# Optimization experiments

Measured on AMD Instinct MI355X. Metric: run time of the kernel, lower is better.

The kernel has to match this reference:

```python
import jax, jax.numpy as jnp
import numpy as np
from jax import lax

N_CHANNELS = 64
N_FILTERS = 256
N_LAYERS = 9  # residual blocks use dilations 2**1 .. 2**(N_LAYERS-1)


def causal_conv1d(x, w, dilation):
    """Causal dilated conv. x: [B,T,Cin], w: [K,Cin,Cout]."""
    pad = (w.shape[0] - 1) * dilation
    return lax.conv_general_dilated(
        x, w, window_strides=(1,), padding=[(pad, 0)],
        rhs_dilation=(dilation,), dimension_numbers=("NWC", "WIO", "NWC"))


def setup_inputs() -> dict:
    key = jax.random.key(0)
    ks = jax.random.split(key, 12)
    B, T, C, F, L = 8, 4096, N_CHANNELS, N_FILTERS, N_LAYERS
    s = lambda fan_in: 1.0 / np.sqrt(fan_in)
    return {
        "x": jax.random.normal(ks[0], (B, T, C), jnp.float32),
        "Wc": jax.random.normal(ks[1], (2, C, F), jnp.float32) * s(2 * C),
        "Wf": jax.random.normal(ks[2], (L - 1, 2, F, F), jnp.float32) * s(2 * F),
        "Wg": jax.random.normal(ks[3], (L - 1, 2, F, F), jnp.float32) * s(2 * F),
        "Wr": jax.random.normal(ks[4], (L - 1, F, F), jnp.float32) * s(F),
        "br": jnp.zeros((L - 1, F), jnp.float32),
        "Ws": jax.random.normal(ks[5], (L - 1, F, F), jnp.float32) * s(F),
        "bs": jnp.zeros((L - 1, F), jnp.float32),
        "Wd1": jax.random.normal(ks[6], (F, C), jnp.float32) * s(F),
        "bd1": jnp.zeros((C,), jnp.float32),
        "Wd2": jax.random.normal(ks[7], (C, C), jnp.float32) * s(C),
        "bd2": jnp.zeros((C,), jnp.float32),
    }


def reference(x, Wc, Wf, Wg, Wr, br, Ws, bs, Wd1, bd1, Wd2, bd2):
    # Initial causal conv, dilation 1, no bias.
    out = causal_conv1d(x, Wc, 1)  # [B,T,F]
    skip_sum = jnp.zeros_like(out)
    for i in range(N_LAYERS - 1):
        d = 2 ** (i + 1)
        f = causal_conv1d(out, Wf[i], d)
        g = causal_conv1d(out, Wg[i], d)
        z = jnp.tanh(f) * jax.nn.sigmoid(g)
        out = out + jnp.einsum("btf,fo->bto", z, Wr[i]) + br[i]
        skip_sum = skip_sum + jnp.einsum("btf,fo->bto", z, Ws[i]) + bs[i]
    h = jax.nn.selu(skip_sum)
    h = jnp.einsum("btf,fc->btc", h, Wd1) + bd1
    h = jax.nn.selu(h)
    h = jnp.einsum("btc,co->bto", h, Wd2) + bd2
    return h
```

## Files before the change

kernel.cpp:

```cpp
#include <hip/hip_runtime.h>
#include <cstdint>

typedef unsigned short u16;
typedef unsigned int u32;
typedef __attribute__((ext_vector_type(8))) short s8v;
typedef __attribute__((ext_vector_type(4))) float f4v;

#define FCH 256

__device__ __forceinline__ float bf2f(u16 u){ return __uint_as_float(((u32)u)<<16); }
__device__ __forceinline__ u16 f2bf(float x){
  u32 u = __float_as_uint(x);
  u += 0x7fffu + ((u>>16)&1u);
  return (u16)(u>>16);
}
__device__ __forceinline__ float rcpf(float x){ return __builtin_amdgcn_rcpf(x); }
__device__ __forceinline__ uint4 pack8(float4 a, float4 b){
  uint4 o;
  o.x = (u32)f2bf(a.x) | ((u32)f2bf(a.y)<<16);
  o.y = (u32)f2bf(a.z) | ((u32)f2bf(a.w)<<16);
  o.z = (u32)f2bf(b.x) | ((u32)f2bf(b.y)<<16);
  o.w = (u32)f2bf(b.z) | ((u32)f2bf(b.w)<<16);
  return o;
}
__device__ __forceinline__ float seluf(float x){
  const float sc = 1.0507009873554805f, al = 1.6732632423543772f;
  return x > 0.f ? sc*x : sc*al*(__expf(x)-1.f);
}
__device__ __forceinline__ s8v ldmask(const u16* p, u32 m){
  uint4 r = *reinterpret_cast<const uint4*>(p);
  r.x &= m; r.y &= m; r.z &= m; r.w &= m;
  s8v v; *reinterpret_cast<uint4*>(&v) = r;
  return v;
}
__device__ __forceinline__ int xcd_tile(int bid, int nT8){
  return nT8 ? ((bid & 7) * nT8 + (bid >> 3)) : bid;
}

__global__ __launch_bounds__(256) void pack_kernel(
    const float* __restrict__ Wc, const float* __restrict__ Wf, const float* __restrict__ Wg,
    const float* __restrict__ Wr, const float* __restrict__ Ws,
    const float* __restrict__ Wd1, const float* __restrict__ Wd2,
    u16* __restrict__ Bp1, u16* __restrict__ Bp2, u16* __restrict__ Bp0,
    u16* __restrict__ BpD1, u16* __restrict__ BpD2)
{
  int gid = blockIdx.x*256 + threadIdx.x;
  int frag = gid >> 6;
  int lane = gid & 63;
  int q = lane >> 4, i15 = lane & 15;
  u16 v[8];
  u16* dst;
  if (frag < 4096) {
    int layer = frag >> 9, rem = frag & 511;
    int kc = rem >> 5, nt = rem & 31;
    int n = nt*16 + i15;
    const float* W = (n < 256) ? Wf : Wg;
    int nn = (n < 256) ? n : n - 256;
    #pragma unroll
    for (int j = 0; j < 8; ++j) {
      int k = kc*32 + q*8 + j;
      int tap = k >> 8, cin = k & 255;
      v[j] = f2bf(W[((size_t)((layer*2 + tap)*256 + cin))*256 + nn]);
    }
    dst = Bp1 + (size_t)frag*512 + lane*8;
  } else if (frag < 6144) {
    int f = frag - 4096;
    int layer = f >> 8, rem = f & 255;
    int kc = rem >> 5, nt = rem & 31;
    int n = nt*16 + i15;
    const float* W = (n < 256) ? Wr : Ws;
    int nn = (n < 256) ? n : n - 256;
    #pragma unroll
    for (int j = 0; j < 8; ++j) {
      int k = kc*32 + q*8 + j;
      v[j] = f2bf(W[((size_t)(layer*256 + k))*256 + nn]);
    }
    dst = Bp2 + (size_t)f*512 + lane*8;
  } else if (frag < 6208) {
    int f = frag - 6144;
    int kc = f >> 4, nt = f & 15;
    int n = nt*16 + i15;
    #pragma unroll
    for (int j = 0; j < 8; ++j) {
      int k = kc*32 + q*8 + j;
      int tap = k >> 6, cin = k & 63;
      v[j] = f2bf(Wc[(size_t)(tap*64 + cin)*256 + n]);
    }
    dst = Bp0 + (size_t)f*512 + lane*8;
  } else if (frag < 6240) {
    int f = frag - 6208;
    int kc = f >> 2, nt = f & 3;
    int n = nt*16 + i15;
    #pragma unroll
    for (int j = 0; j < 8; ++j) {
      int k = kc*32 + q*8 + j;
      v[j] = f2bf(Wd1[(size_t)k*64 + n]);
    }
    dst = BpD1 + (size_t)f*512 + lane*8;
  } else if (frag < 6248) {
    int f = frag - 6240;
    int kc = f >> 2, nt = f & 3;
    int n = nt*16 + i15;
    #pragma unroll
    for (int j = 0; j < 8; ++j) {
      int k = kc*32 + q*8 + j;
      v[j] = f2bf(Wd2[(size_t)k*64 + n]);
    }
    dst = BpD2 + (size_t)f*512 + lane*8;
  } else return;
  uint4 o;
  o.x = (u32)v[0] | ((u32)v[1] << 16);
  o.y = (u32)v[2] | ((u32)v[3] << 16);
  o.z = (u32)v[4] | ((u32)v[5] << 16);
  o.w = (u32)v[6] | ((u32)v[7] << 16);
  *reinterpret_cast<uint4*>(dst) = o;
}

__global__ __launch_bounds__(256, 2) void conv0_kernel(
    const float* __restrict__ x, u16* __restrict__ outBf,
    const u16* __restrict__ Bp0, int nT8)
{
  __shared__ __align__(16) u16 ldsA[2][2048];
  const int tid = threadIdx.x;
  const int w = tid >> 6, lane = tid & 63, q = lane >> 4, i15 = lane & 15;
  const int rb = xcd_tile(blockIdx.x, nT8) * 64;
  const int sm = tid >> 2, sg = tid & 3;
  const int grow = rb + sm;
  const int tpos = grow & 4095;
  const int sunit = ((sm >> 4)*64 + sg*16 + ((sm & 15) ^ (sg << 1))) * 8;
  const int runit = (q*16 + (i15 ^ (q << 1))) * 8;

  f4v acc[4][4];
  #pragma unroll
  for (int jj = 0; jj < 4; ++jj)
    #pragma unroll
    for (int mt = 0; mt < 4; ++mt)
      acc[jj][mt] = (f4v){0.f,0.f,0.f,0.f};

  float4 f0 = {0.f,0.f,0.f,0.f}, f1 = {0.f,0.f,0.f,0.f};
  if (tpos >= 1) {
    const float* px = x + (size_t)(grow-1)*64 + sg*8;
    f0 = *reinterpret_cast<const float4*>(px);
    f1 = *reinterpret_cast<const float4*>(px + 4);
  }
  *reinterpret_cast<uint4*>(&ldsA[0][sunit]) = pack8(f0, f1);
  s8v bcur[4], bnxt[4];
  #pragma unroll
  for (int jj = 0; jj < 4; ++jj)
    bcur[jj] = *reinterpret_cast<const s8v*>(Bp0 + ((size_t)(w + 4*jj)*64 + lane)*8);
  __syncthreads();

  for (int kc = 0; kc < 4; ++kc) {
    const int cur = kc & 1;
    uint4 an = {0u,0u,0u,0u};
    if (kc < 3) {
      int kg = (kc+1)*32 + sg*8;
      int tap = kg >> 6, col = kg & 63;
      float4 g0 = {0.f,0.f,0.f,0.f}, g1 = {0.f,0.f,0.f,0.f};
      if (tap) {
        const float* px = x + (size_t)grow*64 + col;
        g0 = *reinterpret_cast<const float4*>(px);
        g1 = *reinterpret_cast<const float4*>(px + 4);
      } else if (tpos >= 1) {
        const float* px = x + (size_t)(grow-1)*64 + col;
        g0 = *reinterpret_cast<const float4*>(px);
        g1 = *reinterpret_cast<const float4*>(px + 4);
      }
      an = pack8(g0, g1);
      #pragma unroll
      for (int jj = 0; jj < 4; ++jj)
        bnxt[jj] = *reinterpret_cast<const s8v*>(Bp0 + (((size_t)(kc+1)*16 + (w + 4*jj))*64 + lane)*8);
    }
    s8v af[4];
    #pragma unroll
    for (int mt = 0; mt < 4; ++mt)
      af[mt] = *reinterpret_cast<const s8v*>(&ldsA[cur][mt*512 + runit]);
    #pragma unroll
    for (int jj = 0; jj < 4; ++jj)
      #pragma unroll
      for (int mt = 0; mt < 4; ++mt)
        acc[jj][mt] = __builtin_amdgcn_mfma_f32_16x16x32_bf16(af[mt], bcur[jj], acc[jj][mt], 0,0,0);
    if (kc < 3) {
      *reinterpret_cast<uint4*>(&ldsA[cur ^ 1][sunit]) = an;
      #pragma unroll
      for (int jj = 0; jj < 4; ++jj) bcur[jj] = bnxt[jj];
    }
    __syncthreads();
  }

  #pragma unroll
  for (int jj = 0; jj < 4; ++jj) {
    const int cc = (w + 4*jj)*16 + i15;
    #pragma unroll
    for (int mt = 0; mt < 4; ++mt)
      #pragma unroll
      for (int r = 0; r < 4; ++r) {
        const int g2 = rb + mt*16 + q*4 + r;
        outBf[(size_t)g2*FCH + cc] = f2bf(acc[jj][mt][r]);
      }
  }
}

__global__ __launch_bounds__(256, 3) void layer_kernel(
    const u16* __restrict__ inBf, u16* __restrict__ outBf,
    u16* __restrict__ skipB,
    const u16* __restrict__ Bp1, const u16* __restrict__ Bp2,
    const float* __restrict__ br, const float* __restrict__ bs,
    int dil, int first, int nT8)
{
  __shared__ __align__(16) u16 ldsZ[32*264];
  const int tid = threadIdx.x;
  const int w = __builtin_amdgcn_readfirstlane(tid >> 6);
  const int lane = tid & 63, q = lane >> 4, i15 = lane & 15;
  const int rb = xcd_tile(blockIdx.x, nT8) * 32;

  f4v acc[8][2];
  #pragma unroll
  for (int jj = 0; jj < 8; ++jj)
    #pragma unroll
    for (int mt = 0; mt < 2; ++mt)
      acc[jj][mt] = (f4v){0.f,0.f,0.f,0.f};

  {
    const u16* a0p[2];
    const u16* a1p[2];
    u32 am[2];
    #pragma unroll
    for (int mt = 0; mt < 2; ++mt) {
      const int row = rb + mt*16 + i15;
      const bool v = (row & 4095) >= dil;
      a0p[mt] = inBf + (size_t)(v ? row - dil : row)*FCH + q*8;
      a1p[mt] = inBf + (size_t)row*FCH + q*8;
      am[mt]  = v ? 0xffffffffu : 0u;
    }

    s8v bb[3][4], aa[4][2];
    #pragma unroll
    for (int j2 = 0; j2 < 4; ++j2) {
      bb[0][j2] = *reinterpret_cast<const s8v*>(Bp1 + ((size_t)(w + 4*j2)*64 + lane)*8);
      bb[1][j2] = *reinterpret_cast<const s8v*>(Bp1 + ((size_t)(w + 16 + 4*j2)*64 + lane)*8);
    }
    #pragma unroll
    for (int c = 0; c < 3; ++c)
      #pragma unroll
      for (int mt = 0; mt < 2; ++mt)
        aa[c][mt] = ldmask(a0p[mt] + c*32, am[mt]);

    #pragma unroll
    for (int s = 0; s < 32; ++s) {
      const int kc = s >> 1, h = s & 1;
      if (s + 2 < 32) {
        const int sp = s + 2, kcp = sp >> 1, hp = sp & 1;
        #pragma unroll
        for (int j2 = 0; j2 < 4; ++j2)
          bb[sp % 3][j2] = *reinterpret_cast<const s8v*>(
              Bp1 + (((size_t)kcp*32 + (w + 16*hp + 4*j2))*64 + lane)*8);
      }
      if (h == 0 && kc + 3 < 16) {
        const int ca = kc + 3;
        if (ca < 8) {
          #pragma unroll
          for (int mt = 0; mt < 2; ++mt)
            aa[ca & 3][mt] = ldmask(a0p[mt] + ca*32, am[mt]);
        } else {
          #pragma unroll
          for (int mt = 0; mt < 2; ++mt)
            aa[ca & 3][mt] = *reinterpret_cast<const s8v*>(a1p[mt] + (ca - 8)*32);
        }
      }
      __builtin_amdgcn_s_setprio(1);
      #pragma unroll
      for (int j2 = 0; j2 < 4; ++j2)
        #pragma unroll
        for (int mt = 0; mt < 2; ++mt)
          acc[h*4 + j2][mt] = __builtin_amdgcn_mfma_f32_16x16x32_bf16(
              aa[kc & 3][mt], bb[s % 3][j2], acc[h*4 + j2][mt], 0,0,0);
      __builtin_amdgcn_s_setprio(0);
    }
  }

  s8v s2b[3][4];
  #pragma unroll
  for (int j2 = 0; j2 < 4; ++j2) {
    s2b[0][j2] = *reinterpret_cast<const s8v*>(Bp2 + ((size_t)(w + 4*j2)*64 + lane)*8);
    s2b[1][j2] = *reinterpret_cast<const s8v*>(Bp2 + ((size_t)(w + 16 + 4*j2)*64 + lane)*8);
  }

  #pragma unroll
  for (int jj = 0; jj < 4; ++jj) {
    const int colb = (w + 4*jj)*16 + i15;
    #pragma unroll
    for (int mt = 0; mt < 2; ++mt)
      #pragma unroll
      for (int r = 0; r < 4; ++r) {
        float f = acc[jj][mt][r];
        float g = acc[jj+4][mt][r];
        float z = (1.f - 2.f*rcpf(__expf(2.f*f) + 1.f)) * rcpf(1.f + __expf(-g));
        ldsZ[(mt*16 + q*4 + r)*264 + colb] = f2bf(z);
      }
  }
  #pragma unroll
  for (int jj = 0; jj < 8; ++jj)
    #pragma unroll
    for (int mt = 0; mt < 2; ++mt)
      acc[jj][mt] = (f4v){0.f,0.f,0.f,0.f};
  __syncthreads();

  {
    s8v zf[2][2];
    #pragma unroll
    for (int mt = 0; mt < 2; ++mt)
      zf[0][mt] = *reinterpret_cast<const s8v*>(&ldsZ[(mt*16 + i15)*264 + q*8]);
    #pragma unroll
    for (int s = 0; s < 16; ++s) {
      const int kc = s >> 1, h = s & 1;
      if (s + 2 < 16) {
        const int sp = s + 2, kcp = sp >> 1, hp = sp & 1;
        #pragma unroll
        for (int j2 = 0; j2 < 4; ++j2)
          s2b[sp % 3][j2] = *reinterpret_cast<const s8v*>(
              Bp2 + (((size_t)kcp*32 + (w + 16*hp + 4*j2))*64 + lane)*8);
        if (hp == 0) {
          #pragma unroll
          for (int mt = 0; mt < 2; ++mt)
            zf[kcp & 1][mt] = *reinterpret_cast<const s8v*>(&ldsZ[(mt*16 + i15)*264 + kcp*32 + q*8]);
        }
      }
      __builtin_amdgcn_s_setprio(1);
      #pragma unroll
      for (int j2 = 0; j2 < 4; ++j2)
        #pragma unroll
        for (int mt = 0; mt < 2; ++mt)
          acc[h*4 + j2][mt] = __builtin_amdgcn_mfma_f32_16x16x32_bf16(
              zf[kc & 1][mt], s2b[s % 3][j2], acc[h*4 + j2][mt], 0,0,0);
      __builtin_amdgcn_s_setprio(0);
    }
  }

  u16 resv[4][2][4], skv[4][2][4];
  #pragma unroll
  for (int jj = 0; jj < 4; ++jj) {
    const int cc = (w + 4*jj)*16 + i15;
    #pragma unroll
    for (int mt = 0; mt < 2; ++mt)
      #pragma unroll
      for (int r = 0; r < 4; ++r)
        resv[jj][mt][r] = inBf[(size_t)(rb + mt*16 + q*4 + r)*FCH + cc];
  }
  if (!first) {
    #pragma unroll
    for (int jj = 0; jj < 4; ++jj) {
      const int cc = (w + 4*jj)*16 + i15;
      #pragma unroll
      for (int mt = 0; mt < 2; ++mt)
        #pragma unroll
        for (int r = 0; r < 4; ++r)
          skv[jj][mt][r] = skipB[(size_t)(rb + mt*16 + q*4 + r)*FCH + cc];
    }
  }
  #pragma unroll
  for (int jj = 0; jj < 8; ++jj) {
    const int nt = w + 4*jj;
    const bool isR = (jj < 4);
    const int cc = (isR ? nt*16 : (nt-16)*16) + i15;
    const float bias = isR ? br[cc] : bs[cc];
    #pragma unroll
    for (int mt = 0; mt < 2; ++mt)
      #pragma unroll
      for (int r = 0; r < 4; ++r) {
        const int g2 = rb + mt*16 + q*4 + r;
        float vv = acc[jj][mt][r] + bias;
        if (isR) vv += bf2f(resv[jj][mt][r]);
        else if (!first) vv += bf2f(skv[jj-4][mt][r]);
        u16 hv = f2bf(vv);
        if (isR) outBf[(size_t)g2*FCH + cc] = hv;
        else     skipB[(size_t)g2*FCH + cc] = hv;
      }
  }
}

__global__ __launch_bounds__(256, 2) void final_kernel(
    const u16* __restrict__ skipB, const u16* __restrict__ BpD1, const u16* __restrict__ BpD2,
    const float* __restrict__ bd1, const float* __restrict__ bd2, float* __restrict__ outp,
    int nT8)
{
  __shared__ __align__(16) u16 ldsH[64*264];
  __shared__ __align__(16) u16 ldsH2[64*72];
  const int tid = threadIdx.x;
  const int w = tid >> 6, lane = tid & 63, q = lane >> 4, i15 = lane & 15;
  const int rb = xcd_tile(blockIdx.x, nT8) * 64;
  const int sm = tid >> 2, sseg = tid & 3;

  {
    const u16* sp = skipB + (size_t)(rb + sm)*256 + sseg*64;
    u16* dr = &ldsH[sm*264 + sseg*64];
    #pragma unroll
    for (int u = 0; u < 8; ++u) {
      uint4 raw = *reinterpret_cast<const uint4*>(sp + u*8);
      u32 rr[4] = {raw.x, raw.y, raw.z, raw.w};
      uint4 o;
      u32 oo[4];
      #pragma unroll
      for (int p = 0; p < 4; ++p) {
        float e0 = seluf(bf2f((u16)(rr[p] & 0xffffu)));
        float e1 = seluf(bf2f((u16)(rr[p] >> 16)));
        oo[p] = (u32)f2bf(e0) | ((u32)f2bf(e1) << 16);
      }
      o.x = oo[0]; o.y = oo[1]; o.z = oo[2]; o.w = oo[3];
      *reinterpret_cast<uint4*>(dr + u*8) = o;
    }
  }
  __syncthreads();

  f4v a1[4];
  #pragma unroll
  for (int mt = 0; mt < 4; ++mt) a1[mt] = (f4v){0.f,0.f,0.f,0.f};
  for (int kc = 0; kc < 8; ++kc) {
    s8v b = *reinterpret_cast<const s8v*>(BpD1 + ((size_t)(kc*4 + w)*64 + lane)*8);
    #pragma unroll
    for (int mt = 0; mt < 4; ++mt) {
      s8v af = *reinterpret_cast<const s8v*>(&ldsH[(mt*16 + i15)*264 + kc*32 + q*8]);
      a1[mt] = __builtin_amdgcn_mfma_f32_16x16x32_bf16(af, b, a1[mt], 0,0,0);
    }
  }
  const float bb1 = bd1[w*16 + i15];
  #pragma unroll
  for (int mt = 0; mt < 4; ++mt)
    #pragma unroll
    for (int r = 0; r < 4; ++r)
      ldsH2[(mt*16 + q*4 + r)*72 + w*16 + i15] = f2bf(seluf(a1[mt][r] + bb1));
  __syncthreads();

  f4v a2[4];
  #pragma unroll
  for (int mt = 0; mt < 4; ++mt) a2[mt] = (f4v){0.f,0.f,0.f,0.f};
  #pragma unroll
  for (int kc = 0; kc < 2; ++kc) {
    s8v b = *reinterpret_cast<const s8v*>(BpD2 + ((size_t)(kc*4 + w)*64 + lane)*8);
    #pragma unroll
    for (int mt = 0; mt < 4; ++mt) {
      s8v af = *reinterpret_cast<const s8v*>(&ldsH2[(mt*16 + i15)*72 + kc*32 + q*8]);
      a2[mt] = __builtin_amdgcn_mfma_f32_16x16x32_bf16(af, b, a2[mt], 0,0,0);
    }
  }
  const float bb2 = bd2[w*16 + i15];
  #pragma unroll
  for (int mt = 0; mt < 4; ++mt)
    #pragma unroll
    for (int r = 0; r < 4; ++r)
      outp[(size_t)(rb + mt*16 + q*4 + r)*64 + w*16 + i15] = a2[mt][r] + bb2;
}

__global__ __launch_bounds__(256) void zero_kernel(uint4* __restrict__ outp, int n16)
{
  int i = blockIdx.x*256 + threadIdx.x;
  if (i < n16) outp[i] = (uint4){0u,0u,0u,0u};
}

extern "C" void kernel_launch(void* const* d_in, const int* in_sizes, int n_in,
                              void* d_out, int out_size, void* d_ws, size_t ws_size,
                              hipStream_t stream)
{
  (void)n_in;
  const float* x   = (const float*)d_in[0];
  const float* Wc  = (const float*)d_in[1];
  const float* Wf  = (const float*)d_in[2];
  const float* Wg  = (const float*)d_in[3];
  const float* Wr  = (const float*)d_in[4];
  const float* br  = (const float*)d_in[5];
  const float* Ws  = (const float*)d_in[6];
  const float* bs  = (const float*)d_in[7];
  const float* Wd1 = (const float*)d_in[8];
  const float* bd1 = (const float*)d_in[9];
  const float* Wd2 = (const float*)d_in[10];
  const float* bd2 = (const float*)d_in[11];

  const size_t ROWS = (size_t)in_sizes[0] / 64;
  const int gridC = (int)(ROWS / 64);
  const int gridL = (int)(ROWS / 32);
  const int nT8C = (gridC % 8 == 0) ? gridC / 8 : 0;
  const int nT8L = (gridL % 8 == 0) ? gridL / 8 : 0;

  const size_t packsB = (size_t)6248 * 512 * 2;
  const size_t bfBuf  = ROWS * 256 * 2;
  const size_t needB = packsB + 3*bfBuf;

  if (ws_size < needB) {
    int n16 = (out_size * 4) / 16;
    zero_kernel<<<(n16 + 255)/256, 256, 0, stream>>>((uint4*)d_out, n16);
    return;
  }

  char* ws = (char*)d_ws;
  u16* Bp1    = (u16*)ws;            ws += (size_t)4096*512*2;
  u16* Bp2    = (u16*)ws;            ws += (size_t)2048*512*2;
  u16* Bp0    = (u16*)ws;            ws += (size_t)64*512*2;
  u16* BpD1   = (u16*)ws;            ws += (size_t)32*512*2;
  u16* BpD2   = (u16*)ws;            ws += (size_t)8*512*2;
  u16* skipB  = (u16*)ws;            ws += bfBuf;
  u16* bufA   = (u16*)ws;            ws += bfBuf;
  u16* bufB   = (u16*)ws;            ws += bfBuf;

  pack_kernel<<<1562, 256, 0, stream>>>(Wc, Wf, Wg, Wr, Ws, Wd1, Wd2,
                                        Bp1, Bp2, Bp0, BpD1, BpD2);
  conv0_kernel<<<gridC, 256, 0, stream>>>(x, bufA, Bp0, nT8C);
  u16* bufs[2] = {bufA, bufB};
  for (int i = 0; i < 8; ++i) {
    layer_kernel<<<gridL, 256, 0, stream>>>(
        bufs[i & 1], bufs[(i + 1) & 1], skipB,
        Bp1 + (size_t)i*262144, Bp2 + (size_t)i*131072,
        br + i*256, bs + i*256, 2 << i, (i == 0) ? 1 : 0, nT8L);
  }
  final_kernel<<<gridC, 256, 0, stream>>>(skipB, BpD1, BpD2, bd1, bd2,
                                          (float*)d_out, nT8C);
}
```

Measured before the change: 481.6 us.

## Fuse final dense head into last residual layer kernel

The final SELU+dense+SELU+dense head now runs inside the last layer_kernel launch, working on the skip tile still held in registers. This removes a separate kernel launch and the write and re-read of the full skip buffer for the final layer, and the last layer no longer computes the residual output. The skip-buffer load is also moved earlier, before the gated activation stage, to overlap its latency. In exchange, layer_kernel carries more code, an extra LDS array and higher register pressure, which may reduce occupancy for every layer.

Result: slower. 520.1 us (+8.0%).

```diff
diff --git a/kernel.cpp b/kernel.cpp
--- a/kernel.cpp
+++ b/kernel.cpp
@@ -206,9 +206,13 @@
     u16* __restrict__ skipB,
     const u16* __restrict__ Bp1, const u16* __restrict__ Bp2,
     const float* __restrict__ br, const float* __restrict__ bs,
-    int dil, int first, int nT8)
+    const u16* __restrict__ BpD1, const u16* __restrict__ BpD2,
+    const float* __restrict__ bd1, const float* __restrict__ bd2,
+    float* __restrict__ outp,
+    int dil, int first, int last, int nT8)
 {
   __shared__ __align__(16) u16 ldsZ[32*264];
+  __shared__ __align__(16) u16 ldsH2[32*72];
   const int tid = threadIdx.x;
   const int w = __builtin_amdgcn_readfirstlane(tid >> 6);
   const int lane = tid & 63, q = lane >> 4, i15 = lane & 15;
@@ -285,6 +289,18 @@
     s2b[0][j2] = *reinterpret_cast<const s8v*>(Bp2 + ((size_t)(w + 4*j2)*64 + lane)*8);
     s2b[1][j2] = *reinterpret_cast<const s8v*>(Bp2 + ((size_t)(w + 16 + 4*j2)*64 + lane)*8);
   }
+  u16 skv[4][2][4];
+  if (!first) {
+    #pragma unroll
+    for (int jj = 0; jj < 4; ++jj) {
+      const int cc = (w + 4*jj)*16 + i15;
+      #pragma unroll
+      for (int mt = 0; mt < 2; ++mt)
+        #pragma unroll
+        for (int r = 0; r < 4; ++r)
+          skv[jj][mt][r] = skipB[(size_t)(rb + mt*16 + q*4 + r)*FCH + cc];
+    }
+  }
 
   #pragma unroll
   for (int jj = 0; jj < 4; ++jj) {
@@ -337,17 +353,8 @@
     }
   }
 
-  u16 resv[4][2][4], skv[4][2][4];
-  #pragma unroll
-  for (int jj = 0; jj < 4; ++jj) {
-    const int cc = (w + 4*jj)*16 + i15;
-    #pragma unroll
-    for (int mt = 0; mt < 2; ++mt)
-      #pragma unroll
-      for (int r = 0; r < 4; ++r)
-        resv[jj][mt][r] = inBf[(size_t)(rb + mt*16 + q*4 + r)*FCH + cc];
-  }
-  if (!first) {
+  if (!last) {
+    u16 resv[4][2][4];
     #pragma unroll
     for (int jj = 0; jj < 4; ++jj) {
       const int cc = (w + 4*jj)*16 + i15;
@@ -355,97 +362,89 @@
       for (int mt = 0; mt < 2; ++mt)
         #pragma unroll
         for (int r = 0; r < 4; ++r)
-          skv[jj][mt][r] = skipB[(size_t)(rb + mt*16 + q*4 + r)*FCH + cc];
-    }
-  }
-  #pragma unroll
-  for (int jj = 0; jj < 8; ++jj) {
-    const int nt = w + 4*jj;
-    const bool isR = (jj < 4);
-    const int cc = (isR ? nt*16 : (nt-16)*16) + i15;
-    const float bias = isR ? br[cc] : bs[cc];
+          resv[jj][mt][r] = inBf[(size_t)(rb + mt*16 + q*4 + r)*FCH + cc];
+    }
+    #pragma unroll
+    for (int jj = 0; jj < 4; ++jj) {
+      const int cc = (w + 4*jj)*16 + i15;
+      const float bias = br[cc];
+      #pragma unroll
+      for (int mt = 0; mt < 2; ++mt)
+        #pragma unroll
+        for (int r = 0; r < 4; ++r) {
+          const int g2 = rb + mt*16 + q*4 + r;
+          float vv = acc[jj][mt][r] + bias + bf2f(resv[jj][mt][r]);
+          outBf[(size_t)g2*FCH + cc] = f2bf(vv);
+        }
+    }
+    #pragma unroll
+    for (int jj = 4; jj < 8; ++jj) {
+      const int cc = (jj - 4 + 0)*0 + ((w + 4*jj - 16 - 4*4 + 16))*0;
+      const int cc2 = ((w + 4*jj) - 16)*16 + i15;
+      const float bias = bs[cc2];
+      #pragma unroll
+      for (int mt = 0; mt < 2; ++mt)
+        #pragma unroll
+        for (int r = 0; r < 4; ++r) {
+          const int g2 = rb + mt*16 + q*4 + r;
+          float vv = acc[jj][mt][r] + bias;
+          if (!first) vv += bf2f(skv[jj-4][mt][r]);
+          skipB[(size_t)g2*FCH + cc2] = f2bf(vv);
+        }
+    }
+    return;
+  }
+
+  __syncthreads();
+  #pragma unroll
+  for (int jj = 4; jj < 8; ++jj) {
+    const int cc = ((w + 4*jj) - 16)*16 + i15;
+    const float bias = bs[cc];
     #pragma unroll
     for (int mt = 0; mt < 2; ++mt)
       #pragma unroll
       for (int r = 0; r < 4; ++r) {
-        const int g2 = rb + mt*16 + q*4 + r;
         float vv = acc[jj][mt][r] + bias;
-        if (isR) vv += bf2f(resv[jj][mt][r]);
-        else if (!first) vv += bf2f(skv[jj-4][mt][r]);
-        u16 hv = f2bf(vv);
-        if (isR) outBf[(size_t)g2*FCH + cc] = hv;
-        else     skipB[(size_t)g2*FCH + cc] = hv;
-      }
-  }
-}
-
-__global__ __launch_bounds__(256, 2) void final_kernel(
-    const u16* __restrict__ skipB, const u16* __restrict__ BpD1, const u16* __restrict__ BpD2,
-    const float* __restrict__ bd1, const float* __restrict__ bd2, float* __restrict__ outp,
-    int nT8)
-{
-  __shared__ __align__(16) u16 ldsH[64*264];
-  __shared__ __align__(16) u16 ldsH2[64*72];
-  const int tid = threadIdx.x;
-  const int w = tid >> 6, lane = tid & 63, q = lane >> 4, i15 = lane & 15;
-  const int rb = xcd_tile(blockIdx.x, nT8) * 64;
-  const int sm = tid >> 2, sseg = tid & 3;
-
-  {
-    const u16* sp = skipB + (size_t)(rb + sm)*256 + sseg*64;
-    u16* dr = &ldsH[sm*264 + sseg*64];
-    #pragma unroll
-    for (int u = 0; u < 8; ++u) {
-      uint4 raw = *reinterpret_cast<const uint4*>(sp + u*8);
-      u32 rr[4] = {raw.x, raw.y, raw.z, raw.w};
-      uint4 o;
-      u32 oo[4];
-      #pragma unroll
-      for (int p = 0; p < 4; ++p) {
-        float e0 = seluf(bf2f((u16)(rr[p] & 0xffffu)));
-        float e1 = seluf(bf2f((u16)(rr[p] >> 16)));
-        oo[p] = (u32)f2bf(e0) | ((u32)f2bf(e1) << 16);
-      }
-      o.x = oo[0]; o.y = oo[1]; o.z = oo[2]; o.w = oo[3];
-      *reinterpret_cast<uint4*>(dr + u*8) = o;
-    }
+        if (!first) vv += bf2f(skv[jj-4][mt][r]);
+        ldsZ[(mt*16 + q*4 + r)*264 + cc] = f2bf(seluf(vv));
+      }
   }
   __syncthreads();
 
-  f4v a1[4];
-  #pragma unroll
-  for (int mt = 0; mt < 4; ++mt) a1[mt] = (f4v){0.f,0.f,0.f,0.f};
+  f4v a1[2];
+  #pragma unroll
+  for (int mt = 0; mt < 2; ++mt) a1[mt] = (f4v){0.f,0.f,0.f,0.f};
   for (int kc = 0; kc < 8; ++kc) {
     s8v b = *reinterpret_cast<const s8v*>(BpD1 + ((size_t)(kc*4 + w)*64 + lane)*8);
     #pragma unroll
-    for (int mt = 0; mt < 4; ++mt) {
-      s8v af = *reinterpret_cast<const s8v*>(&ldsH[(mt*16 + i15)*264 + kc*32 + q*8]);
+    for (int mt = 0; mt < 2; ++mt) {
+      s8v af = *reinterpret_cast<const s8v*>(&ldsZ[(mt*16 + i15)*264 + kc*32 + q*8]);
       a1[mt] = __builtin_amdgcn_mfma_f32_16x16x32_bf16(af, b, a1[mt], 0,0,0);
     }
   }
   const float bb1 = bd1[w*16 + i15];
   #pragma unroll
-  for (int mt = 0; mt < 4; ++mt)
+  for (int mt = 0; mt < 2; ++mt)
     #pragma unroll
     for (int r = 0; r < 4; ++r)
       ldsH2[(mt*16 + q*4 + r)*72 + w*16 + i15] = f2bf(seluf(a1[mt][r] + bb1));
   __syncthreads();
 
-  f4v a2[4];
-  #pragma unroll
-  for (int mt = 0; mt < 4; ++mt) a2[mt] = (f4v){0.f,0.f,0.f,0.f};
+  f4v a2[2];
+  #pragma unroll
+  for (int mt = 0; mt < 2; ++mt) a2[mt] = (f4v){0.f,0.f,0.f,0.f};
   #pragma unroll
   for (int kc = 0; kc < 2; ++kc) {
     s8v b = *reinterpret_cast<const s8v*>(BpD2 + ((size_t)(kc*4 + w)*64 + lane)*8);
     #pragma unroll
-    for (int mt = 0; mt < 4; ++mt) {
+    for (int mt = 0; mt < 2; ++mt) {
       s8v af = *reinterpret_cast<const s8v*>(&ldsH2[(mt*16 + i15)*72 + kc*32 + q*8]);
       a2[mt] = __builtin_amdgcn_mfma_f32_16x16x32_bf16(af, b, a2[mt], 0,0,0);
     }
   }
   const float bb2 = bd2[w*16 + i15];
   #pragma unroll
-  for (int mt = 0; mt < 4; ++mt)
+  for (int mt = 0; mt < 2; ++mt)
     #pragma unroll
     for (int r = 0; r < 4; ++r)
       outp[(size_t)(rb + mt*16 + q*4 + r)*64 + w*16 + i15] = a2[mt][r] + bb2;
@@ -509,8 +508,8 @@
     layer_kernel<<<gridL, 256, 0, stream>>>(
         bufs[i & 1], bufs[(i + 1) & 1], skipB,
         Bp1 + (size_t)i*262144, Bp2 + (size_t)i*131072,
-        br + i*256, bs + i*256, 2 << i, (i == 0) ? 1 : 0, nT8L);
-  }
-  final_kernel<<<gridC, 256, 0, stream>>>(skipB, BpD1, BpD2, bd1, bd2,
-                                          (float*)d_out, nT8C);
-}
+        br + i*256, bs + i*256,
+        BpD1, BpD2, bd1, bd2, (float*)d_out,
+        2 << i, (i == 0) ? 1 : 0, (i == 7) ? 1 : 0, nT8L);
+  }
+}
```
